# Optimization experiments

Measured on AMD Instinct MI355X. Metric: run time of the kernel, lower is better.

## Reference

```python
import jax, jax.numpy as jnp
import numpy as np

QLEN, BSZ, D_MODEL = 2048, 2, 1024
N_HEAD, D_HEAD = 16, 64
SCALE = 1.0 / (D_HEAD ** 0.5)
LN_EPS = 1e-5


def _rel_shift(x):
    # x: [qlen, klen, bsz, n_head]
    q, k, b, n = x.shape
    zero_pad = jnp.zeros((q, 1, b, n), dtype=x.dtype)
    x_padded = jnp.concatenate([zero_pad, x], axis=1).reshape(k + 1, q, b, n)
    return x_padded[1:].reshape(q, k, b, n)


def setup_inputs() -> dict:
    key = jax.random.key(0)
    ks = jax.random.split(key, 6)
    w = jax.random.normal(ks[0], (QLEN, BSZ, D_MODEL), dtype=jnp.float32)
    r_emb = jax.random.normal(ks[1], (QLEN, N_HEAD, D_HEAD), dtype=jnp.float32) * 0.02
    r_w_bias = jax.random.normal(ks[2], (N_HEAD, D_HEAD), dtype=jnp.float32) * 0.02
    r_bias = jax.random.normal(ks[3], (QLEN, N_HEAD), dtype=jnp.float32) * 0.02
    # causal mask (1 above diagonal => masked), dim==2 branch of original forward
    attn_mask = jnp.triu(jnp.ones((QLEN, QLEN), dtype=jnp.float32), k=1)
    W_qkv = jax.random.normal(ks[4], (D_MODEL, 3 * N_HEAD * D_HEAD), dtype=jnp.float32) * (D_MODEL ** -0.5)
    W_o = jax.random.normal(ks[5], (N_HEAD * D_HEAD, D_MODEL), dtype=jnp.float32) * (D_MODEL ** -0.5)
    ln_g = jnp.ones((D_MODEL,), dtype=jnp.float32)
    ln_b = jnp.zeros((D_MODEL,), dtype=jnp.float32)
    return {"w": w, "r_emb": r_emb, "r_w_bias": r_w_bias, "r_bias": r_bias,
            "attn_mask": attn_mask, "W_qkv": W_qkv, "W_o": W_o, "ln_g": ln_g, "ln_b": ln_b}


def reference(w, r_emb, r_w_bias, r_bias, attn_mask, W_qkv, W_o, ln_g, ln_b):
    qlen, bsz, d_model = w.shape
    n_head, d_head = r_w_bias.shape

    w_heads = w @ W_qkv                                   # [q, b, 3*n*d]
    q_h, k_h, v_h = jnp.split(w_heads, 3, axis=-1)
    q_h = q_h.reshape(qlen, bsz, n_head, d_head)
    k_h = k_h.reshape(qlen, bsz, n_head, d_head)
    v_h = v_h.reshape(qlen, bsz, n_head, d_head)
    klen = k_h.shape[0]

    # klen == r_emb.size(0) here, so slicing is a no-op (kept for fidelity)
    r_emb_s = r_emb[-klen:]
    r_bias_s = r_bias[-klen:]

    rw_head_q = q_h + r_w_bias[None, None]                # [q, b, n, d]
    AC = jnp.einsum('ibnd,jbnd->ijbn', rw_head_q, k_h)    # content-content
    B_ = jnp.einsum('ibnd,jnd->ijbn', q_h, r_emb_s)       # content-position
    D_ = r_bias_s[None, :, None, :]                       # [1, k, 1, n]
    BD = _rel_shift(B_ + D_)

    attn_score = (AC + BD) * SCALE
    attn_score = attn_score + attn_mask[:, :, None, None] * (-1e9)
    attn_prob = jax.nn.softmax(attn_score, axis=1)

    attn_vec = jnp.einsum('ijbn,jbnd->ibnd', attn_prob, v_h)
    attn_vec = attn_vec.reshape(qlen, bsz, n_head * d_head)
    attn_out = attn_vec @ W_o

    # residual + LayerNorm
    y = w + attn_out
    mu = jnp.mean(y, axis=-1, keepdims=True)
    var = jnp.var(y, axis=-1, keepdims=True)
    return (y - mu) / jnp.sqrt(var + LN_EPS) * ln_g + ln_b
```

## Files before the change

kernel.cpp:

```cpp
#include <hip/hip_runtime.h>

typedef unsigned short ushort_t;
typedef unsigned short us4 __attribute__((ext_vector_type(4)));
typedef unsigned short us8 __attribute__((ext_vector_type(8)));
typedef unsigned int   u32x4 __attribute__((ext_vector_type(4)));
typedef float          f32x4 __attribute__((ext_vector_type(4)));
typedef __bf16         bf16x8 __attribute__((ext_vector_type(8)));

__device__ __forceinline__ unsigned short f2bf(float f) {
  unsigned u = __builtin_bit_cast(unsigned, f);
  u += 0x7fffu + ((u >> 16) & 1u);
  return (unsigned short)(u >> 16);
}
__device__ __forceinline__ float bf2f(unsigned short h) {
  unsigned u = ((unsigned)h) << 16;
  return __builtin_bit_cast(float, u);
}


__global__ __launch_bounds__(256) void k_conv_x(const float* __restrict__ in,
                                                ushort_t* __restrict__ out) {
  int i = (blockIdx.x * 256 + threadIdx.x) * 4;
  float4 v = *(const float4*)(in + i);
  us4 o;
  o[0] = f2bf(v.x); o[1] = f2bf(v.y); o[2] = f2bf(v.z); o[3] = f2bf(v.w);
  *(us4*)(out + i) = o;
}

__global__ __launch_bounds__(256) void k_transpose_bf16(const float* __restrict__ in,
                                                        ushort_t* __restrict__ out,
                                                        int R, int C) {
  __shared__ float tile[32][33];
  int c0 = blockIdx.x * 32, r0 = blockIdx.y * 32;
  int tx = threadIdx.x, ty = threadIdx.y;
#pragma unroll
  for (int k = 0; k < 32; k += 8)
    tile[ty + k][tx] = in[(size_t)(r0 + ty + k) * C + c0 + tx];
  __syncthreads();
#pragma unroll
  for (int k = 0; k < 32; k += 8)
    out[(size_t)(c0 + ty + k) * R + r0 + tx] = f2bf(tile[tx][ty + k]);
}

__global__ __launch_bounds__(256) void k_conv_remb(const float* __restrict__ re,
                                                   ushort_t* __restrict__ out) {
  int tid = blockIdx.x * 256 + threadIdx.x;
  int o = tid * 8;
  int d = o & 63, r = (o >> 6) & 2047, h = o >> 17;
  const float* src = re + ((size_t)r * 16 + h) * 64 + d;
  float4 a = *(const float4*)(src);
  float4 b = *(const float4*)(src + 4);
  us8 u;
  u[0] = f2bf(a.x); u[1] = f2bf(a.y); u[2] = f2bf(a.z); u[3] = f2bf(a.w);
  u[4] = f2bf(b.x); u[5] = f2bf(b.y); u[6] = f2bf(b.z); u[7] = f2bf(b.w);
  *(us8*)(out + o) = u;
}

__global__ __launch_bounds__(256) void k_rbias2(const ushort_t* __restrict__ RE,
                                                const float* __restrict__ rwb,
                                                const float* __restrict__ rbias,
                                                float* __restrict__ out) {
  int tid = blockIdx.x * 256 + threadIdx.x;
  int h = tid >> 11, r = tid & 2047;
  const ushort_t* re = RE + ((size_t)h * 2048 + r) * 64;
  const float* wv = rwb + h * 64;
  float acc = 0.f;
#pragma unroll
  for (int d0 = 0; d0 < 64; d0 += 8) {
    us8 v = *(const us8*)(re + d0);
#pragma unroll
    for (int e = 0; e < 8; ++e) acc += bf2f(v[e]) * wv[d0 + e];
  }
  out[h * 2048 + r] = (rbias[r * 16 + h] - acc) * 0.125f;
}


__global__ __launch_bounds__(256) void k_gemm_qkv(const ushort_t* __restrict__ A,
                                                  const ushort_t* __restrict__ B,
                                                  const float* __restrict__ rwb,
                                                  ushort_t* __restrict__ qt,
                                                  ushort_t* __restrict__ kk,
                                                  ushort_t* __restrict__ vv) {
  __shared__ ushort_t Al[128 * 32], Bl[128 * 32];
  int row0 = blockIdx.x * 128, col0 = blockIdx.y * 128;
  int t = threadIdx.x, w = t >> 6, l = t & 63;
  int wr = w >> 1, wc = w & 1, g = l >> 4, cl = l & 15;
  f32x4 acc[4][4];
#pragma unroll
  for (int m = 0; m < 4; ++m)
#pragma unroll
    for (int n = 0; n < 4; ++n) acc[m][n] = (f32x4){0.f, 0.f, 0.f, 0.f};
  for (int k0 = 0; k0 < 1024; k0 += 32) {
#pragma unroll
    for (int c = 0; c < 2; ++c) {
      int u = t + 256 * c, row = u >> 2, col = (u & 3) * 8;
      *(u32x4*)(&Al[row * 32 + col]) = *(const u32x4*)(A + (size_t)(row0 + row) * 1024 + k0 + col);
      *(u32x4*)(&Bl[row * 32 + col]) = *(const u32x4*)(B + (size_t)(col0 + row) * 1024 + k0 + col);
    }
    __syncthreads();
    bf16x8 af[4], bfr[4];
#pragma unroll
    for (int m = 0; m < 4; ++m) af[m] = *(const bf16x8*)(&Al[(wr * 64 + m * 16 + cl) * 32 + g * 8]);
#pragma unroll
    for (int n = 0; n < 4; ++n) bfr[n] = *(const bf16x8*)(&Bl[(wc * 64 + n * 16 + cl) * 32 + g * 8]);
#pragma unroll
    for (int m = 0; m < 4; ++m)
#pragma unroll
      for (int n = 0; n < 4; ++n)
        acc[m][n] = __builtin_amdgcn_mfma_f32_16x16x32_bf16(af[m], bfr[n], acc[m][n], 0, 0, 0);
    __syncthreads();
  }
  int sec = col0 >> 10;
#pragma unroll
  for (int m = 0; m < 4; ++m) {
#pragma unroll
    for (int n = 0; n < 4; ++n) {
#pragma unroll
      for (int r = 0; r < 4; ++r) {
        int row = row0 + wr * 64 + m * 16 + g * 4 + r;
        int col = col0 + wc * 64 + n * 16 + cl;
        int mm = col & 1023, hh = mm >> 6, d = mm & 63;
        int bq = row & 1, iq = row >> 1;
        float val = acc[m][n][r];
        if (sec == 0) {
          qt[(((size_t)bq * 16 + hh) * 2048 + iq) * 64 + d] = f2bf((val + rwb[mm]) * 0.125f);
        } else if (sec == 1) {
          kk[(((size_t)bq * 16 + hh) * 2048 + iq) * 64 + d] = f2bf(val);
        } else {
          vv[(((size_t)bq * 16 + hh) * 64 + d) * 2048 + iq] = f2bf(val);
        }
      }
    }
  }
}


__global__ __launch_bounds__(256, 3) void k_flash(const ushort_t* __restrict__ QT,
                                                  const ushort_t* __restrict__ KK,
                                                  const ushort_t* __restrict__ VT,
                                                  const ushort_t* __restrict__ RE,
                                                  const float* __restrict__ RB2,
                                                  ushort_t* __restrict__ AV) {
  int bh = blockIdx.x, b = bh >> 4, h = bh & 15;
  int i0 = (gridDim.y - 1 - blockIdx.y) * 64;
  int t = threadIdx.x, w = t >> 6, l = t & 63, g = l >> 4, cl = l & 15;

  __shared__ ushort_t Klds[64 * 72];
  __shared__ ushort_t Vt[64 * 72];
  __shared__ ushort_t Rl[128 * 72];
  __shared__ float rb2s[128];
  __shared__ ushort_t Pls[4][16 * 72];
  __shared__ float alphal[4][16];
  __shared__ float lsuml[4][16];

  const ushort_t* qb = QT + ((size_t)(b * 16 + h)) * 2048 * 64;
  const ushort_t* kb = KK + ((size_t)(b * 16 + h)) * 2048 * 64;
  const ushort_t* vt = VT + ((size_t)(b * 16 + h)) * 64 * 2048;
  const ushort_t* rbase = RE + (size_t)h * 2048 * 64;
  const float* r2 = RB2 + h * 2048;

  int qrow = i0 + w * 16 + cl;
  bf16x8 qa0 = *(const bf16x8*)(qb + (size_t)qrow * 64 + g * 8);
  bf16x8 qa1 = *(const bf16x8*)(qb + (size_t)qrow * 64 + 32 + g * 8);

  float m_run[4], l_run[4];
  f32x4 Ot[4];
#pragma unroll
  for (int r = 0; r < 4; ++r) { m_run[r] = -1e30f; l_run[r] = 0.f; }
#pragma unroll
  for (int dt = 0; dt < 4; ++dt) Ot[dt] = (f32x4){0.f, 0.f, 0.f, 0.f};

  int nt = gridDim.y - blockIdx.y;
  int rb0f = 1984 - i0;
  int urow = t >> 3, ucol = (t & 7) * 8;

  *(u32x4*)(&Rl[((rb0f + urow) & 127) * 72 + ucol]) =
      *(const u32x4*)(rbase + (size_t)(rb0f + urow) * 64 + ucol);
  *(u32x4*)(&Rl[((rb0f + urow + 32) & 127) * 72 + ucol]) =
      *(const u32x4*)(rbase + (size_t)(rb0f + urow + 32) * 64 + ucol);
  if (t < 64) rb2s[(rb0f + t) & 127] = r2[rb0f + t];

  u32x4 kreg0, kreg1, vreg0, vreg1, rreg0, rreg1;
  float rb2reg;

  {
    int j0n = 0;
    kreg0 = *(const u32x4*)(kb + (size_t)(j0n + urow) * 64 + ucol);
    kreg1 = *(const u32x4*)(kb + (size_t)(j0n + urow + 32) * 64 + ucol);
    vreg0 = *(const u32x4*)(vt + (size_t)urow * 2048 + j0n + ucol);
    vreg1 = *(const u32x4*)(vt + (size_t)(urow + 32) * 2048 + j0n + ucol);
    int gs = rb0f + 64;
    int rr0 = gs + urow, rr1 = gs + urow + 32;
    rreg0 = (rr0 < 2048) ? *(const u32x4*)(rbase + (size_t)rr0 * 64 + ucol) : (u32x4){0u, 0u, 0u, 0u};
    rreg1 = (rr1 < 2048) ? *(const u32x4*)(rbase + (size_t)rr1 * 64 + ucol) : (u32x4){0u, 0u, 0u, 0u};
    int rrb = gs + t;
    rb2reg = (t < 64 && rrb < 2048) ? r2[rrb] : 0.f;
  }

  for (int tt = 0; tt < nt; ++tt) {
    int j0 = tt * 64;
    int rb0 = rb0f + j0;
    __syncthreads();
    {
      *(u32x4*)(&Klds[urow * 72 + ucol]) = kreg0;
      *(u32x4*)(&Klds[(urow + 32) * 72 + ucol]) = kreg1;
      *(u32x4*)(&Vt[urow * 72 + ucol]) = vreg0;
      *(u32x4*)(&Vt[(urow + 32) * 72 + ucol]) = vreg1;
      int gs = rb0 + 64;
      *(u32x4*)(&Rl[((gs + urow) & 127) * 72 + ucol]) = rreg0;
      *(u32x4*)(&Rl[((gs + urow + 32) & 127) * 72 + ucol]) = rreg1;
      if (t < 64) rb2s[(gs + t) & 127] = rb2reg;
    }
    __syncthreads();
    if (tt + 1 < nt) {
      int j0n = j0 + 64;
      kreg0 = *(const u32x4*)(kb + (size_t)(j0n + urow) * 64 + ucol);
      kreg1 = *(const u32x4*)(kb + (size_t)(j0n + urow + 32) * 64 + ucol);
      vreg0 = *(const u32x4*)(vt + (size_t)urow * 2048 + j0n + ucol);
      vreg1 = *(const u32x4*)(vt + (size_t)(urow + 32) * 2048 + j0n + ucol);
      int gs = rb0f + j0n + 64;
      int rr0 = gs + urow, rr1 = gs + urow + 32;
      rreg0 = (rr0 < 2048) ? *(const u32x4*)(rbase + (size_t)rr0 * 64 + ucol) : (u32x4){0u, 0u, 0u, 0u};
      rreg1 = (rr1 < 2048) ? *(const u32x4*)(rbase + (size_t)rr1 * 64 + ucol) : (u32x4){0u, 0u, 0u, 0u};
      int rrb = gs + t;
      rb2reg = (t < 64 && rrb < 2048) ? r2[rrb] : 0.f;
    }

    int bw0 = 48 - 16 * w;
    int rB = rb0 + bw0;
    f32x4 bwf[5];
#pragma unroll
    for (int ct = 0; ct < 5; ++ct) {
      int prow = (rB + ct * 16) & 127;
      f32x4 a = (f32x4){0.f, 0.f, 0.f, 0.f};
      bf16x8 rr0 = *(const bf16x8*)(&Rl[(prow + cl) * 72 + g * 8]);
      a = __builtin_amdgcn_mfma_f32_16x16x32_bf16(qa0, rr0, a, 0, 0, 0);
      bf16x8 rr1 = *(const bf16x8*)(&Rl[(prow + cl) * 72 + 32 + g * 8]);
      a = __builtin_amdgcn_mfma_f32_16x16x32_bf16(qa1, rr1, a, 0, 0, 0);
      float rv = rb2s[(prow + cl) & 127];
      a[0] += rv; a[1] += rv; a[2] += rv; a[3] += rv;
      bwf[ct] = a;
    }

    f32x4 S[4];
#pragma unroll
    for (int ct = 0; ct < 4; ++ct) {
      f32x4 a = (f32x4){0.f, 0.f, 0.f, 0.f};
      bf16x8 kf0 = *(const bf16x8*)(&Klds[(ct * 16 + cl) * 72 + g * 8]);
      a = __builtin_amdgcn_mfma_f32_16x16x32_bf16(qa0, kf0, a, 0, 0, 0);
      bf16x8 kf1 = *(const bf16x8*)(&Klds[(ct * 16 + cl) * 72 + 32 + g * 8]);
      a = __builtin_amdgcn_mfma_f32_16x16x32_bf16(qa1, kf1, a, 0, 0, 0);
      S[ct] = a;
    }

    int climit = i0 - j0 + 15 + 16 * w;
#pragma unroll
    for (int r = 0; r < 4; ++r) {
      int rl = g * 4 + r;
      int dlt = cl - rl + 15;
      int src = (l & 48) | (dlt & 15);
      float b0 = __shfl(bwf[0][r], src);
      float b1 = __shfl(bwf[1][r], src);
      float b2 = __shfl(bwf[2][r], src);
      float b3 = __shfl(bwf[3][r], src);
      float b4 = __shfl(bwf[4][r], src);
      if (dlt >= 16) { b0 = b1; b1 = b2; b2 = b3; b3 = b4; }
      float sv[4];
      sv[0] = (dlt      <= climit) ? S[0][r] + b0 : -1e30f;
      sv[1] = (dlt + 16 <= climit) ? S[1][r] + b1 : -1e30f;
      sv[2] = (dlt + 32 <= climit) ? S[2][r] + b2 : -1e30f;
      sv[3] = (dlt + 48 <= climit) ? S[3][r] + b3 : -1e30f;
      float rmax = fmaxf(fmaxf(sv[0], sv[1]), fmaxf(sv[2], sv[3]));
      rmax = fmaxf(rmax, __shfl_xor(rmax, 1));
      rmax = fmaxf(rmax, __shfl_xor(rmax, 2));
      rmax = fmaxf(rmax, __shfl_xor(rmax, 4));
      rmax = fmaxf(rmax, __shfl_xor(rmax, 8));
      float mn = fmaxf(m_run[r], rmax);
      float al = __expf(m_run[r] - mn);
      m_run[r] = mn;
      float rsum = 0.f;
#pragma unroll
      for (int ct = 0; ct < 4; ++ct) {
        float pv = __expf(sv[ct] - mn);
        sv[ct] = pv;
        rsum += pv;
      }
      rsum += __shfl_xor(rsum, 1);
      rsum += __shfl_xor(rsum, 2);
      rsum += __shfl_xor(rsum, 4);
      rsum += __shfl_xor(rsum, 8);
      l_run[r] = l_run[r] * al + rsum;
      if (cl == 0) alphal[w][rl] = al;
#pragma unroll
      for (int ct = 0; ct < 4; ++ct)
        Pls[w][rl * 72 + ct * 16 + cl] = f2bf(sv[ct]);
    }
    __syncthreads();

    float aq = alphal[w][cl];
    bf16x8 pb0 = *(const bf16x8*)(&Pls[w][cl * 72 + g * 8]);
    bf16x8 pb1 = *(const bf16x8*)(&Pls[w][cl * 72 + 32 + g * 8]);
#pragma unroll
    for (int dt = 0; dt < 4; ++dt) {
      f32x4 o = Ot[dt];
      o[0] *= aq; o[1] *= aq; o[2] *= aq; o[3] *= aq;
      bf16x8 va0 = *(const bf16x8*)(&Vt[(dt * 16 + cl) * 72 + g * 8]);
      o = __builtin_amdgcn_mfma_f32_16x16x32_bf16(va0, pb0, o, 0, 0, 0);
      bf16x8 va1 = *(const bf16x8*)(&Vt[(dt * 16 + cl) * 72 + 32 + g * 8]);
      o = __builtin_amdgcn_mfma_f32_16x16x32_bf16(va1, pb1, o, 0, 0, 0);
      Ot[dt] = o;
    }
  }

  if (cl == 0) {
#pragma unroll
    for (int r = 0; r < 4; ++r) lsuml[w][g * 4 + r] = l_run[r];
  }
  float inv = 1.f / lsuml[w][cl];
  int orow = (i0 + w * 16 + cl) * 2 + b;
#pragma unroll
  for (int dt = 0; dt < 4; ++dt) {
    us4 o4;
    o4[0] = f2bf(Ot[dt][0] * inv);
    o4[1] = f2bf(Ot[dt][1] * inv);
    o4[2] = f2bf(Ot[dt][2] * inv);
    o4[3] = f2bf(Ot[dt][3] * inv);
    *(us4*)(&AV[(size_t)orow * 1024 + h * 64 + dt * 16 + g * 4]) = o4;
  }
}


__global__ __launch_bounds__(256) void k_gemm_o(const ushort_t* __restrict__ A,
                                                const ushort_t* __restrict__ B,
                                                const float* __restrict__ wsrc,
                                                float* __restrict__ Y) {
  __shared__ ushort_t Al[128 * 32], Bl[128 * 32];
  int row0 = blockIdx.x * 128, col0 = blockIdx.y * 128;
  int t = threadIdx.x, w = t >> 6, l = t & 63;
  int wr = w >> 1, wc = w & 1, g = l >> 4, cl = l & 15;
  f32x4 acc[4][4];
#pragma unroll
  for (int m = 0; m < 4; ++m)
#pragma unroll
    for (int n = 0; n < 4; ++n) acc[m][n] = (f32x4){0.f, 0.f, 0.f, 0.f};
  for (int k0 = 0; k0 < 1024; k0 += 32) {
#pragma unroll
    for (int c = 0; c < 2; ++c) {
      int u = t + 256 * c, row = u >> 2, col = (u & 3) * 8;
      *(u32x4*)(&Al[row * 32 + col]) = *(const u32x4*)(A + (size_t)(row0 + row) * 1024 + k0 + col);
      *(u32x4*)(&Bl[row * 32 + col]) = *(const u32x4*)(B + (size_t)(col0 + row) * 1024 + k0 + col);
    }
    __syncthreads();
    bf16x8 af[4], bfr[4];
#pragma unroll
    for (int m = 0; m < 4; ++m) af[m] = *(const bf16x8*)(&Al[(wr * 64 + m * 16 + cl) * 32 + g * 8]);
#pragma unroll
    for (int n = 0; n < 4; ++n) bfr[n] = *(const bf16x8*)(&Bl[(wc * 64 + n * 16 + cl) * 32 + g * 8]);
#pragma unroll
    for (int m = 0; m < 4; ++m)
#pragma unroll
      for (int n = 0; n < 4; ++n)
        acc[m][n] = __builtin_amdgcn_mfma_f32_16x16x32_bf16(af[m], bfr[n], acc[m][n], 0, 0, 0);
    __syncthreads();
  }
#pragma unroll
  for (int m = 0; m < 4; ++m) {
#pragma unroll
    for (int n = 0; n < 4; ++n) {
#pragma unroll
      for (int r = 0; r < 4; ++r) {
        int row = row0 + wr * 64 + m * 16 + g * 4 + r;
        int col = col0 + wc * 64 + n * 16 + cl;
        size_t idx = (size_t)row * 1024 + col;
        Y[idx] = acc[m][n][r] + wsrc[idx];
      }
    }
  }
}


__global__ __launch_bounds__(256) void k_ln(const float* __restrict__ Y,
                                            const float* __restrict__ gg,
                                            const float* __restrict__ bb,
                                            float* __restrict__ out) {
  int row = blockIdx.x, t = threadIdx.x;
  float4 v = *(const float4*)(Y + (size_t)row * 1024 + t * 4);
  float s = v.x + v.y + v.z + v.w;
  float q = v.x * v.x + v.y * v.y + v.z * v.z + v.w * v.w;
#pragma unroll
  for (int m = 32; m >= 1; m >>= 1) {
    s += __shfl_xor(s, m);
    q += __shfl_xor(q, m);
  }
  __shared__ float ssh[4], qsh[4];
  int w = t >> 6, l = t & 63;
  if (l == 0) { ssh[w] = s; qsh[w] = q; }
  __syncthreads();
  s = ssh[0] + ssh[1] + ssh[2] + ssh[3];
  q = qsh[0] + qsh[1] + qsh[2] + qsh[3];
  float mu = s * (1.f / 1024.f);
  float var = q * (1.f / 1024.f) - mu * mu;
  float rstd = rsqrtf(var + 1e-5f);
  float4 gv = *(const float4*)(gg + t * 4);
  float4 bv = *(const float4*)(bb + t * 4);
  float4 o;
  o.x = (v.x - mu) * rstd * gv.x + bv.x;
  o.y = (v.y - mu) * rstd * gv.y + bv.y;
  o.z = (v.z - mu) * rstd * gv.z + bv.z;
  o.w = (v.w - mu) * rstd * gv.w + bv.w;
  *(float4*)(out + (size_t)row * 1024 + t * 4) = o;
}


extern "C" void kernel_launch(void* const* d_in, const int* in_sizes, int n_in,
                              void* d_out, int out_size, void* d_ws, size_t ws_size,
                              hipStream_t stream) {
  const float* w      = (const float*)d_in[0];
  const float* r_emb  = (const float*)d_in[1];
  const float* r_w_b  = (const float*)d_in[2];
  const float* r_bias = (const float*)d_in[3];
  const float* W_qkv  = (const float*)d_in[5];
  const float* W_o    = (const float*)d_in[6];
  const float* ln_g   = (const float*)d_in[7];
  const float* ln_b   = (const float*)d_in[8];
  float* out = (float*)d_out;
  char* ws = (char*)d_ws;

  ushort_t* X16  = (ushort_t*)(ws + 0);
  ushort_t* WQ16 = (ushort_t*)(ws + 8388608);
  ushort_t* WO16 = (ushort_t*)(ws + 14680064);
  ushort_t* RE16 = (ushort_t*)(ws + 16777216);
  float*    RB2  = (float*)(ws + 20971520);
  ushort_t* QT16 = (ushort_t*)(ws + 21102592);
  ushort_t* K16  = (ushort_t*)(ws + 29491200);
  ushort_t* VT16 = (ushort_t*)(ws + 37879808);
  ushort_t* AV16 = (ushort_t*)(ws + 46268416);
  float*    Y32  = (float*)(ws + 54657024);

  k_conv_x<<<4096, 256, 0, stream>>>(w, X16);
  k_transpose_bf16<<<dim3(96, 32), dim3(32, 8), 0, stream>>>(W_qkv, WQ16, 1024, 3072);
  k_transpose_bf16<<<dim3(32, 32), dim3(32, 8), 0, stream>>>(W_o, WO16, 1024, 1024);
  k_conv_remb<<<1024, 256, 0, stream>>>(r_emb, RE16);
  k_rbias2<<<128, 256, 0, stream>>>(RE16, r_w_b, r_bias, RB2);
  k_gemm_qkv<<<dim3(32, 24), 256, 0, stream>>>(X16, WQ16, r_w_b, QT16, K16, VT16);
  k_flash<<<dim3(32, 32), 256, 0, stream>>>(QT16, K16, VT16, RE16, RB2, AV16);
  k_gemm_o<<<dim3(32, 8), 256, 0, stream>>>(AV16, WO16, w, Y32);
  k_ln<<<4096, 256, 0, stream>>>(Y32, ln_g, ln_b, out);
}
```

Before: 201.2 us.

## Use direct global-to-LDS loads, swizzle GEMM blocks, trim flash masking and sync

The QKV and output GEMMs now copy tiles straight from global memory into LDS with global_load_lds and remap block indices into a swizzled 1D grid, aiming for fewer register round-trips and better L2 reuse. In the flash kernel, causal masking runs only on the diagonal tile, s_setprio raises wave priority around the MFMA sections, and one __syncthreads after writing the P tile is removed. Removing that barrier relies on each wave reading only its own Pls/alphal slice, which holds here but leaves intra-wave LDS ordering to the compiler.

```diff
diff --git a/kernel.cpp b/kernel.cpp
--- a/kernel.cpp
+++ b/kernel.cpp
@@ -15,6 +15,12 @@
 __device__ __forceinline__ float bf2f(unsigned short h) {
   unsigned u = ((unsigned)h) << 16;
   return __builtin_bit_cast(float, u);
+}
+
+__device__ __forceinline__ void async_cp16(const ushort_t* g, ushort_t* l) {
+  __builtin_amdgcn_global_load_lds(
+      (const __attribute__((address_space(1))) unsigned int*)g,
+      (__attribute__((address_space(3))) unsigned int*)l, 16, 0, 0);
 }
 
 
@@ -82,7 +88,9 @@
                                                   ushort_t* __restrict__ kk,
                                                   ushort_t* __restrict__ vv) {
   __shared__ ushort_t Al[128 * 32], Bl[128 * 32];
-  int row0 = blockIdx.x * 128, col0 = blockIdx.y * 128;
+  int bid = blockIdx.x;
+  int swz = (bid & 7) * 96 + (bid >> 3);
+  int row0 = (swz & 31) * 128, col0 = (swz >> 5) * 128;
   int t = threadIdx.x, w = t >> 6, l = t & 63;
   int wr = w >> 1, wc = w & 1, g = l >> 4, cl = l & 15;
   f32x4 acc[4][4];
@@ -94,8 +102,8 @@
 #pragma unroll
     for (int c = 0; c < 2; ++c) {
       int u = t + 256 * c, row = u >> 2, col = (u & 3) * 8;
-      *(u32x4*)(&Al[row * 32 + col]) = *(const u32x4*)(A + (size_t)(row0 + row) * 1024 + k0 + col);
-      *(u32x4*)(&Bl[row * 32 + col]) = *(const u32x4*)(B + (size_t)(col0 + row) * 1024 + k0 + col);
+      async_cp16(A + (size_t)(row0 + row) * 1024 + k0 + col, &Al[u * 8]);
+      async_cp16(B + (size_t)(col0 + row) * 1024 + k0 + col, &Bl[u * 8]);
     }
     __syncthreads();
     bf16x8 af[4], bfr[4];
@@ -229,6 +237,7 @@
     int bw0 = 48 - 16 * w;
     int rB = rb0 + bw0;
     f32x4 bwf[5];
+    __builtin_amdgcn_s_setprio(1);
 #pragma unroll
     for (int ct = 0; ct < 5; ++ct) {
       int prow = (rB + ct * 16) & 127;
@@ -252,7 +261,9 @@
       a = __builtin_amdgcn_mfma_f32_16x16x32_bf16(qa1, kf1, a, 0, 0, 0);
       S[ct] = a;
     }
-
+    __builtin_amdgcn_s_setprio(0);
+
+    bool diag = (tt == nt - 1);
     int climit = i0 - j0 + 15 + 16 * w;
 #pragma unroll
     for (int r = 0; r < 4; ++r) {
@@ -266,10 +277,17 @@
       float b4 = __shfl(bwf[4][r], src);
       if (dlt >= 16) { b0 = b1; b1 = b2; b2 = b3; b3 = b4; }
       float sv[4];
-      sv[0] = (dlt      <= climit) ? S[0][r] + b0 : -1e30f;
-      sv[1] = (dlt + 16 <= climit) ? S[1][r] + b1 : -1e30f;
-      sv[2] = (dlt + 32 <= climit) ? S[2][r] + b2 : -1e30f;
-      sv[3] = (dlt + 48 <= climit) ? S[3][r] + b3 : -1e30f;
+      if (diag) {
+        sv[0] = (dlt      <= climit) ? S[0][r] + b0 : -1e30f;
+        sv[1] = (dlt + 16 <= climit) ? S[1][r] + b1 : -1e30f;
+        sv[2] = (dlt + 32 <= climit) ? S[2][r] + b2 : -1e30f;
+        sv[3] = (dlt + 48 <= climit) ? S[3][r] + b3 : -1e30f;
+      } else {
+        sv[0] = S[0][r] + b0;
+        sv[1] = S[1][r] + b1;
+        sv[2] = S[2][r] + b2;
+        sv[3] = S[3][r] + b3;
+      }
       float rmax = fmaxf(fmaxf(sv[0], sv[1]), fmaxf(sv[2], sv[3]));
       rmax = fmaxf(rmax, __shfl_xor(rmax, 1));
       rmax = fmaxf(rmax, __shfl_xor(rmax, 2));
@@ -295,11 +313,11 @@
       for (int ct = 0; ct < 4; ++ct)
         Pls[w][rl * 72 + ct * 16 + cl] = f2bf(sv[ct]);
     }
-    __syncthreads();
 
     float aq = alphal[w][cl];
     bf16x8 pb0 = *(const bf16x8*)(&Pls[w][cl * 72 + g * 8]);
     bf16x8 pb1 = *(const bf16x8*)(&Pls[w][cl * 72 + 32 + g * 8]);
+    __builtin_amdgcn_s_setprio(1);
 #pragma unroll
     for (int dt = 0; dt < 4; ++dt) {
       f32x4 o = Ot[dt];
@@ -310,6 +328,7 @@
       o = __builtin_amdgcn_mfma_f32_16x16x32_bf16(va1, pb1, o, 0, 0, 0);
       Ot[dt] = o;
     }
+    __builtin_amdgcn_s_setprio(0);
   }
 
   if (cl == 0) {
@@ -335,7 +354,9 @@
                                                 const float* __restrict__ wsrc,
                                                 float* __restrict__ Y) {
   __shared__ ushort_t Al[128 * 32], Bl[128 * 32];
-  int row0 = blockIdx.x * 128, col0 = blockIdx.y * 128;
+  int bid = blockIdx.x;
+  int swz = (bid & 7) * 32 + (bid >> 3);
+  int row0 = (swz & 31) * 128, col0 = (swz >> 5) * 128;
   int t = threadIdx.x, w = t >> 6, l = t & 63;
   int wr = w >> 1, wc = w & 1, g = l >> 4, cl = l & 15;
   f32x4 acc[4][4];
@@ -347,8 +368,8 @@
 #pragma unroll
     for (int c = 0; c < 2; ++c) {
       int u = t + 256 * c, row = u >> 2, col = (u & 3) * 8;
-      *(u32x4*)(&Al[row * 32 + col]) = *(const u32x4*)(A + (size_t)(row0 + row) * 1024 + k0 + col);
-      *(u32x4*)(&Bl[row * 32 + col]) = *(const u32x4*)(B + (size_t)(col0 + row) * 1024 + k0 + col);
+      async_cp16(A + (size_t)(row0 + row) * 1024 + k0 + col, &Al[u * 8]);
+      async_cp16(B + (size_t)(col0 + row) * 1024 + k0 + col, &Bl[u * 8]);
     }
     __syncthreads();
     bf16x8 af[4], bfr[4];
@@ -442,8 +463,8 @@
   k_transpose_bf16<<<dim3(32, 32), dim3(32, 8), 0, stream>>>(W_o, WO16, 1024, 1024);
   k_conv_remb<<<1024, 256, 0, stream>>>(r_emb, RE16);
   k_rbias2<<<128, 256, 0, stream>>>(RE16, r_w_b, r_bias, RB2);
-  k_gemm_qkv<<<dim3(32, 24), 256, 0, stream>>>(X16, WQ16, r_w_b, QT16, K16, VT16);
+  k_gemm_qkv<<<768, 256, 0, stream>>>(X16, WQ16, r_w_b, QT16, K16, VT16);
   k_flash<<<dim3(32, 32), 256, 0, stream>>>(QT16, K16, VT16, RE16, RB2, AV16);
-  k_gemm_o<<<dim3(32, 8), 256, 0, stream>>>(AV16, WO16, w, Y32);
+  k_gemm_o<<<256, 256, 0, stream>>>(AV16, WO16, w, Y32);
   k_ln<<<4096, 256, 0, stream>>>(Y32, ln_g, ln_b, out);
 }
```

New measurement: 205.1 us. No clear change (+1.9%).
